# Performance work log

Hardware: AMD Instinct MI355X
Metric: run time of the kernel (lower is better)

## Reference

```python
import jax, jax.numpy as jnp
import numpy as np

TEMPERATURE = 8.0  # sqrt(d_k) with d_k = 64


def setup_inputs() -> dict:
    key = jax.random.key(0)
    k1, k2, k3, k4 = jax.random.split(key, 4)
    B, S, D = 16, 2048, 64  # B = batch * n_heads
    q = jax.random.normal(k1, (B, S, D), dtype=jnp.float32)
    k = jax.random.normal(k2, (B, S, D), dtype=jnp.float32)
    v = jax.random.normal(k3, (B, S, D), dtype=jnp.float32)
    # boolean mask: True = masked out. Low prob so no row is fully masked.
    mask = jax.random.uniform(k4, (B, S, S)) < 0.1
    return {"q": q, "k": k, "v": v, "mask": mask}


def reference(q, k, v, mask):
    # attn = (q @ k^T) / temperature, masked_fill(mask, -inf), softmax over last dim
    attn = jnp.einsum("bqd,bkd->bqk", q, k) / TEMPERATURE
    attn = jnp.where(mask, -jnp.inf, attn)
    attn = jax.nn.softmax(attn, axis=2)
    output = jnp.einsum("bqk,bkd->bqd", attn, v)
    return output, attn
```

## Files before the change

kernel.cpp:

```cpp
#include <hip/hip_runtime.h>

typedef _Float16 half8 __attribute__((ext_vector_type(8)));
typedef _Float16 half4 __attribute__((ext_vector_type(4)));
typedef float    floatx4 __attribute__((ext_vector_type(4)));
typedef int      intx4  __attribute__((ext_vector_type(4)));

#define NB  16
#define SEQ 2048
#define DIM 64

#define MFMA(a,b,c) __builtin_amdgcn_mfma_f32_16x16x32_f16((a),(b),(c),0,0,0)

__global__ __launch_bounds__(256) void cvt_qk_kernel(const float* __restrict__ q,
                                                     const float* __restrict__ k,
                                                     _Float16* __restrict__ qh,
                                                     _Float16* __restrict__ kh) {
    size_t i = ((size_t)blockIdx.x * 256 + threadIdx.x) * 4;
    float4 a = *(const float4*)(q + i);
    float4 b = *(const float4*)(k + i);
    half4 ha = { (_Float16)a.x, (_Float16)a.y, (_Float16)a.z, (_Float16)a.w };
    half4 hb = { (_Float16)b.x, (_Float16)b.y, (_Float16)b.z, (_Float16)b.w };
    *(half4*)(qh + i) = ha;
    *(half4*)(kh + i) = hb;
}

__global__ __launch_bounds__(256) void cvt_vt_kernel(const float* __restrict__ v,
                                                     _Float16* __restrict__ vt) {
    __shared__ float tile[64][65];
    const int b  = blockIdx.x >> 5;
    const int s0 = (blockIdx.x & 31) << 6;
    const int t  = threadIdx.x;
    {
        const int row = t >> 2;
        const int c0  = (t & 3) << 4;
        const float* src = v + ((size_t)(b * SEQ + s0 + row)) * DIM + c0;
        #pragma unroll
        for (int i = 0; i < 4; ++i) {
            float4 x = *(const float4*)(src + i * 4);
            tile[row][c0 + i*4 + 0] = x.x;
            tile[row][c0 + i*4 + 1] = x.y;
            tile[row][c0 + i*4 + 2] = x.z;
            tile[row][c0 + i*4 + 3] = x.w;
        }
    }
    __syncthreads();
    {
        const int d  = t >> 2;
        const int sb = (t & 3) << 4;
        _Float16* dst = vt + ((size_t)(b * DIM + d)) * SEQ + s0 + sb;
        #pragma unroll
        for (int i = 0; i < 4; ++i) {
            half4 h = { (_Float16)tile[sb + i*4 + 0][d],
                        (_Float16)tile[sb + i*4 + 1][d],
                        (_Float16)tile[sb + i*4 + 2][d],
                        (_Float16)tile[sb + i*4 + 3][d] };
            *(half4*)(dst + i*4) = h;
        }
    }
}

__global__ __launch_bounds__(256, 4) void attn_kernel(
    const _Float16* __restrict__ qh, const _Float16* __restrict__ kh,
    const _Float16* __restrict__ vt, const int* __restrict__ mask,
    float* __restrict__ out, float* __restrict__ attn)
{
    __shared__ float wsum[4][16];
    __shared__ __align__(16) _Float16 tsc[4][16][40];
    __shared__ __align__(16) float outred[4][16][68];

    const int b    = blockIdx.x >> 7;
    const int r0   = (blockIdx.x & 127) << 4;
    const int lane = threadIdx.x & 63;
    const int wave = threadIdx.x >> 6;
    const int rl   = lane & 15;
    const int g    = lane >> 4;

    const size_t qoff = ((size_t)(b * SEQ + r0 + rl)) * DIM + g * 8;
    const half8 qa0 = *(const half8*)(qh + qoff);
    const half8 qa1 = *(const half8*)(qh + qoff + 32);

    const _Float16* kbase = kh + (size_t)b * SEQ * DIM + (size_t)rl * DIM + g * 8;
    const int*      mbase = mask + ((size_t)(b * SEQ + r0 + rl)) * SEQ + g * 4;

    float rs = 0.f;
    uint32_t mb0 = 0, mb1 = 0, mb2 = 0, mb3 = 0;

    intx4 pm0 = __builtin_nontemporal_load((const intx4*)(mbase + wave * 32));
    intx4 pm1 = __builtin_nontemporal_load((const intx4*)(mbase + wave * 32 + 16));

    for (int cc = 0; cc < 16; ++cc) {
        const int jj = (cc * 4 + wave) * 32;
        const intx4 m0 = pm0, m1 = pm1;
        if (cc < 15) {
            pm0 = __builtin_nontemporal_load((const intx4*)(mbase + jj + 128));
            pm1 = __builtin_nontemporal_load((const intx4*)(mbase + jj + 128 + 16));
        }
        const _Float16* kp = kbase + (size_t)jj * DIM;
        half8 ka0 = *(const half8*)(kp);
        half8 ka1 = *(const half8*)(kp + 32);
        half8 kb0 = *(const half8*)(kp + 16 * DIM);
        half8 kb1 = *(const half8*)(kp + 16 * DIM + 32);
        floatx4 c0 = {0.f,0.f,0.f,0.f}, c1 = {0.f,0.f,0.f,0.f};
        c0 = MFMA(ka0, qa0, c0);
        c0 = MFMA(ka1, qa1, c0);
        c1 = MFMA(kb0, qa0, c1);
        c1 = MFMA(kb1, qa1, c1);
        float e0 = m0.x ? 0.f : __expf(c0[0] * 0.125f);
        float e1 = m0.y ? 0.f : __expf(c0[1] * 0.125f);
        float e2 = m0.z ? 0.f : __expf(c0[2] * 0.125f);
        float e3 = m0.w ? 0.f : __expf(c0[3] * 0.125f);
        float e4 = m1.x ? 0.f : __expf(c1[0] * 0.125f);
        float e5 = m1.y ? 0.f : __expf(c1[1] * 0.125f);
        float e6 = m1.z ? 0.f : __expf(c1[2] * 0.125f);
        float e7 = m1.w ? 0.f : __expf(c1[3] * 0.125f);
        rs += (e0 + e1) + (e2 + e3) + (e4 + e5) + (e6 + e7);
        uint32_t byt = (m0.x ? 1u : 0u)        | ((m0.y ? 1u : 0u) << 1)
                     | ((m0.z ? 1u : 0u) << 2) | ((m0.w ? 1u : 0u) << 3)
                     | ((m1.x ? 1u : 0u) << 4) | ((m1.y ? 1u : 0u) << 5)
                     | ((m1.z ? 1u : 0u) << 6) | ((m1.w ? 1u : 0u) << 7);
        mb0 = (mb0 >> 8) | (mb1 << 24);
        mb1 = (mb1 >> 8) | (mb2 << 24);
        mb2 = (mb2 >> 8) | (mb3 << 24);
        mb3 = (mb3 >> 8) | (byt << 24);
    }

    rs += __shfl_xor(rs, 16);
    rs += __shfl_xor(rs, 32);
    if (g == 0) wsum[wave][rl] = rs;
    __syncthreads();
    const float inv = 1.0f / (wsum[0][rl] + wsum[1][rl] + wsum[2][rl] + wsum[3][rl]);

    floatx4 o0 = {0.f,0.f,0.f,0.f}, o1 = {0.f,0.f,0.f,0.f};
    floatx4 o2 = {0.f,0.f,0.f,0.f}, o3 = {0.f,0.f,0.f,0.f};
    const _Float16* vbase = vt + ((size_t)b * DIM + rl) * SEQ + g * 8;
    float* abase = attn + ((size_t)(b * SEQ + r0 + rl)) * SEQ + g * 4;

    for (int cc = 0; cc < 16; ++cc) {
        const int jj = (cc * 4 + wave) * 32;
        const _Float16* kp = kbase + (size_t)jj * DIM;
        half8 ka0 = *(const half8*)(kp);
        half8 ka1 = *(const half8*)(kp + 32);
        half8 kb0 = *(const half8*)(kp + 16 * DIM);
        half8 kb1 = *(const half8*)(kp + 16 * DIM + 32);
        floatx4 c0 = {0.f,0.f,0.f,0.f}, c1 = {0.f,0.f,0.f,0.f};
        c0 = MFMA(ka0, qa0, c0);
        c0 = MFMA(ka1, qa1, c0);
        c1 = MFMA(kb0, qa0, c1);
        c1 = MFMA(kb1, qa1, c1);

        const uint32_t byt = mb0 & 0xffu;
        mb0 = (mb0 >> 8) | (mb1 << 24);
        mb1 = (mb1 >> 8) | (mb2 << 24);
        mb2 = (mb2 >> 8) | (mb3 << 24);
        mb3 =  mb3 >> 8;

        float e0 = (byt & 1u)   ? 0.f : __expf(c0[0] * 0.125f);
        float e1 = (byt & 2u)   ? 0.f : __expf(c0[1] * 0.125f);
        float e2 = (byt & 4u)   ? 0.f : __expf(c0[2] * 0.125f);
        float e3 = (byt & 8u)   ? 0.f : __expf(c0[3] * 0.125f);
        float e4 = (byt & 16u)  ? 0.f : __expf(c1[0] * 0.125f);
        float e5 = (byt & 32u)  ? 0.f : __expf(c1[1] * 0.125f);
        float e6 = (byt & 64u)  ? 0.f : __expf(c1[2] * 0.125f);
        float e7 = (byt & 128u) ? 0.f : __expf(c1[3] * 0.125f);

        floatx4 a0 = { e0 * inv, e1 * inv, e2 * inv, e3 * inv };
        floatx4 a1 = { e4 * inv, e5 * inv, e6 * inv, e7 * inv };
        __builtin_nontemporal_store(a0, (floatx4*)(abase + jj));
        __builtin_nontemporal_store(a1, (floatx4*)(abase + jj + 16));

        half4 h0 = { (_Float16)e0, (_Float16)e1, (_Float16)e2, (_Float16)e3 };
        half4 h1 = { (_Float16)e4, (_Float16)e5, (_Float16)e6, (_Float16)e7 };
        *(half4*)(&tsc[wave][rl][g * 4])      = h0;
        *(half4*)(&tsc[wave][rl][16 + g * 4]) = h1;
        half8 eb = *(const half8*)(&tsc[wave][rl][g * 8]);

        const _Float16* vp = vbase + jj;
        half8 v0 = *(const half8*)(vp);
        half8 v1 = *(const half8*)(vp + 16 * SEQ);
        half8 v2 = *(const half8*)(vp + 32 * SEQ);
        half8 v3 = *(const half8*)(vp + 48 * SEQ);
        o0 = MFMA(v0, eb, o0);
        o1 = MFMA(v1, eb, o1);
        o2 = MFMA(v2, eb, o2);
        o3 = MFMA(v3, eb, o3);
    }

    *(floatx4*)(&outred[wave][rl][ 0 + g * 4]) = o0;
    *(floatx4*)(&outred[wave][rl][16 + g * 4]) = o1;
    *(floatx4*)(&outred[wave][rl][32 + g * 4]) = o2;
    *(floatx4*)(&outred[wave][rl][48 + g * 4]) = o3;
    __syncthreads();
    {
        const int r  = threadIdx.x >> 4;
        const int c4 = (threadIdx.x & 15) << 2;
        floatx4 s0 = *(const floatx4*)(&outred[0][r][c4]);
        floatx4 s1 = *(const floatx4*)(&outred[1][r][c4]);
        floatx4 s2 = *(const floatx4*)(&outred[2][r][c4]);
        floatx4 s3 = *(const floatx4*)(&outred[3][r][c4]);
        floatx4 s = (s0 + s1) + (s2 + s3);
        const float inv2 = 1.0f / (wsum[0][r] + wsum[1][r] + wsum[2][r] + wsum[3][r]);
        floatx4 ov = { s[0] * inv2, s[1] * inv2, s[2] * inv2, s[3] * inv2 };
        *(floatx4*)(out + ((size_t)(b * SEQ + r0 + r)) * DIM + c4) = ov;
    }
}

extern "C" void kernel_launch(void* const* d_in, const int* in_sizes, int n_in,
                              void* d_out, int out_size, void* d_ws, size_t ws_size,
                              hipStream_t stream) {
    const float* q = (const float*)d_in[0];
    const float* k = (const float*)d_in[1];
    const float* v = (const float*)d_in[2];
    const int* mask = (const int*)d_in[3];

    float* out  = (float*)d_out;
    float* attn = out + (size_t)NB * SEQ * DIM;

    _Float16* qh = (_Float16*)d_ws;
    _Float16* kh = qh + (size_t)NB * SEQ * DIM;
    _Float16* vt = kh + (size_t)NB * SEQ * DIM;

    cvt_qk_kernel<<<(NB * SEQ * DIM) / 1024, 256, 0, stream>>>(q, k, qh, kh);
    cvt_vt_kernel<<<NB * (SEQ / 64), 256, 0, stream>>>(v, vt);
    attn_kernel<<<NB * (SEQ / 16), 256, 0, stream>>>(qh, kh, vt, mask, out, attn);
}
```

Measured before the change: 652.9 us.

## Pack mask into bitfields in a prepass and raise attention kernel occupancy

Adds a mask_bits_kernel that reads the int32 mask once and packs it with wave ballots into 32-bit words, one bit per key column. The attention kernel then reads those compact words in both passes, replacing the per-thread int4 mask loads and the register shift chain that carried mask bits from pass one to pass two. The attention kernel also aliases its two shared-memory arrays into one buffer, adding a barrier before reuse, so it can ask for 8 blocks per CU instead of 4. The attn stores switch from nontemporal to normal stores. The cost is an extra kernel launch and a separate full pass over the mask, and total mask traffic stays roughly the same.

```diff
diff --git a/kernel.cpp b/kernel.cpp
--- a/kernel.cpp
+++ b/kernel.cpp
@@ -3,7 +3,6 @@
 typedef _Float16 half8 __attribute__((ext_vector_type(8)));
 typedef _Float16 half4 __attribute__((ext_vector_type(4)));
 typedef float    floatx4 __attribute__((ext_vector_type(4)));
-typedef int      intx4  __attribute__((ext_vector_type(4)));
 
 #define NB  16
 #define SEQ 2048
@@ -59,14 +58,32 @@
     }
 }
 
-__global__ __launch_bounds__(256, 4) void attn_kernel(
+__global__ __launch_bounds__(256) void mask_bits_kernel(const int* __restrict__ mask,
+                                                        unsigned int* __restrict__ bits) {
+    const int wave = threadIdx.x >> 6;
+    const int lane = threadIdx.x & 63;
+    const size_t row = (size_t)blockIdx.x * 4 + wave;
+    const int* mp = mask + row * SEQ + lane;
+    unsigned int keep = 0;
+    #pragma unroll
+    for (int it = 0; it < 32; ++it) {
+        int m = __builtin_nontemporal_load(mp + it * 64);
+        unsigned long long bal = __ballot(m != 0);
+        unsigned int half = (lane & 1) ? (unsigned int)(bal >> 32) : (unsigned int)bal;
+        if ((lane >> 1) == it) keep = half;
+    }
+    bits[row * 64 + lane] = keep;
+}
+
+__global__ __launch_bounds__(256, 8) void attn_kernel(
     const _Float16* __restrict__ qh, const _Float16* __restrict__ kh,
-    const _Float16* __restrict__ vt, const int* __restrict__ mask,
+    const _Float16* __restrict__ vt, const unsigned int* __restrict__ bits,
     float* __restrict__ out, float* __restrict__ attn)
 {
     __shared__ float wsum[4][16];
-    __shared__ __align__(16) _Float16 tsc[4][16][40];
-    __shared__ __align__(16) float outred[4][16][68];
+    __shared__ __align__(16) unsigned char lds_u[4 * 16 * 68 * 4];
+    _Float16* tsc    = (_Float16*)lds_u;
+    float*    outred = (float*)lds_u;
 
     const int b    = blockIdx.x >> 7;
     const int r0   = (blockIdx.x & 127) << 4;
@@ -80,21 +97,15 @@
     const half8 qa1 = *(const half8*)(qh + qoff + 32);
 
     const _Float16* kbase = kh + (size_t)b * SEQ * DIM + (size_t)rl * DIM + g * 8;
-    const int*      mbase = mask + ((size_t)(b * SEQ + r0 + rl)) * SEQ + g * 4;
+    const unsigned int* bbase = bits + ((size_t)(b * SEQ + r0 + rl)) * 64 + wave;
 
     float rs = 0.f;
-    uint32_t mb0 = 0, mb1 = 0, mb2 = 0, mb3 = 0;
-
-    intx4 pm0 = __builtin_nontemporal_load((const intx4*)(mbase + wave * 32));
-    intx4 pm1 = __builtin_nontemporal_load((const intx4*)(mbase + wave * 32 + 16));
+    unsigned int pb = bbase[0];
 
     for (int cc = 0; cc < 16; ++cc) {
         const int jj = (cc * 4 + wave) * 32;
-        const intx4 m0 = pm0, m1 = pm1;
-        if (cc < 15) {
-            pm0 = __builtin_nontemporal_load((const intx4*)(mbase + jj + 128));
-            pm1 = __builtin_nontemporal_load((const intx4*)(mbase + jj + 128 + 16));
-        }
+        const unsigned int bm = pb;
+        if (cc < 15) pb = bbase[(cc + 1) * 4];
         const _Float16* kp = kbase + (size_t)jj * DIM;
         half8 ka0 = *(const half8*)(kp);
         half8 ka1 = *(const half8*)(kp + 32);
@@ -105,23 +116,17 @@
         c0 = MFMA(ka1, qa1, c0);
         c1 = MFMA(kb0, qa0, c1);
         c1 = MFMA(kb1, qa1, c1);
-        float e0 = m0.x ? 0.f : __expf(c0[0] * 0.125f);
-        float e1 = m0.y ? 0.f : __expf(c0[1] * 0.125f);
-        float e2 = m0.z ? 0.f : __expf(c0[2] * 0.125f);
-        float e3 = m0.w ? 0.f : __expf(c0[3] * 0.125f);
-        float e4 = m1.x ? 0.f : __expf(c1[0] * 0.125f);
-        float e5 = m1.y ? 0.f : __expf(c1[1] * 0.125f);
-        float e6 = m1.z ? 0.f : __expf(c1[2] * 0.125f);
-        float e7 = m1.w ? 0.f : __expf(c1[3] * 0.125f);
+        const unsigned int blo = bm >> (g * 4);
+        const unsigned int bhi = bm >> (g * 4 + 16);
+        float e0 = (blo & 1u) ? 0.f : __expf(c0[0] * 0.125f);
+        float e1 = (blo & 2u) ? 0.f : __expf(c0[1] * 0.125f);
+        float e2 = (blo & 4u) ? 0.f : __expf(c0[2] * 0.125f);
+        float e3 = (blo & 8u) ? 0.f : __expf(c0[3] * 0.125f);
+        float e4 = (bhi & 1u) ? 0.f : __expf(c1[0] * 0.125f);
+        float e5 = (bhi & 2u) ? 0.f : __expf(c1[1] * 0.125f);
+        float e6 = (bhi & 4u) ? 0.f : __expf(c1[2] * 0.125f);
+        float e7 = (bhi & 8u) ? 0.f : __expf(c1[3] * 0.125f);
         rs += (e0 + e1) + (e2 + e3) + (e4 + e5) + (e6 + e7);
-        uint32_t byt = (m0.x ? 1u : 0u)        | ((m0.y ? 1u : 0u) << 1)
-                     | ((m0.z ? 1u : 0u) << 2) | ((m0.w ? 1u : 0u) << 3)
-                     | ((m1.x ? 1u : 0u) << 4) | ((m1.y ? 1u : 0u) << 5)
-                     | ((m1.z ? 1u : 0u) << 6) | ((m1.w ? 1u : 0u) << 7);
-        mb0 = (mb0 >> 8) | (mb1 << 24);
-        mb1 = (mb1 >> 8) | (mb2 << 24);
-        mb2 = (mb2 >> 8) | (mb3 << 24);
-        mb3 = (mb3 >> 8) | (byt << 24);
     }
 
     rs += __shfl_xor(rs, 16);
@@ -134,9 +139,11 @@
     floatx4 o2 = {0.f,0.f,0.f,0.f}, o3 = {0.f,0.f,0.f,0.f};
     const _Float16* vbase = vt + ((size_t)b * DIM + rl) * SEQ + g * 8;
     float* abase = attn + ((size_t)(b * SEQ + r0 + rl)) * SEQ + g * 4;
+    _Float16* trow = tsc + (wave * 16 + rl) * 40;
 
     for (int cc = 0; cc < 16; ++cc) {
         const int jj = (cc * 4 + wave) * 32;
+        const unsigned int bm = bbase[cc * 4];
         const _Float16* kp = kbase + (size_t)jj * DIM;
         half8 ka0 = *(const half8*)(kp);
         half8 ka1 = *(const half8*)(kp + 32);
@@ -148,31 +155,27 @@
         c1 = MFMA(kb0, qa0, c1);
         c1 = MFMA(kb1, qa1, c1);
 
-        const uint32_t byt = mb0 & 0xffu;
-        mb0 = (mb0 >> 8) | (mb1 << 24);
-        mb1 = (mb1 >> 8) | (mb2 << 24);
-        mb2 = (mb2 >> 8) | (mb3 << 24);
-        mb3 =  mb3 >> 8;
-
-        float e0 = (byt & 1u)   ? 0.f : __expf(c0[0] * 0.125f);
-        float e1 = (byt & 2u)   ? 0.f : __expf(c0[1] * 0.125f);
-        float e2 = (byt & 4u)   ? 0.f : __expf(c0[2] * 0.125f);
-        float e3 = (byt & 8u)   ? 0.f : __expf(c0[3] * 0.125f);
-        float e4 = (byt & 16u)  ? 0.f : __expf(c1[0] * 0.125f);
-        float e5 = (byt & 32u)  ? 0.f : __expf(c1[1] * 0.125f);
-        float e6 = (byt & 64u)  ? 0.f : __expf(c1[2] * 0.125f);
-        float e7 = (byt & 128u) ? 0.f : __expf(c1[3] * 0.125f);
+        const unsigned int blo = bm >> (g * 4);
+        const unsigned int bhi = bm >> (g * 4 + 16);
+        float e0 = (blo & 1u) ? 0.f : __expf(c0[0] * 0.125f);
+        float e1 = (blo & 2u) ? 0.f : __expf(c0[1] * 0.125f);
+        float e2 = (blo & 4u) ? 0.f : __expf(c0[2] * 0.125f);
+        float e3 = (blo & 8u) ? 0.f : __expf(c0[3] * 0.125f);
+        float e4 = (bhi & 1u) ? 0.f : __expf(c1[0] * 0.125f);
+        float e5 = (bhi & 2u) ? 0.f : __expf(c1[1] * 0.125f);
+        float e6 = (bhi & 4u) ? 0.f : __expf(c1[2] * 0.125f);
+        float e7 = (bhi & 8u) ? 0.f : __expf(c1[3] * 0.125f);
 
         floatx4 a0 = { e0 * inv, e1 * inv, e2 * inv, e3 * inv };
         floatx4 a1 = { e4 * inv, e5 * inv, e6 * inv, e7 * inv };
-        __builtin_nontemporal_store(a0, (floatx4*)(abase + jj));
-        __builtin_nontemporal_store(a1, (floatx4*)(abase + jj + 16));
+        *(floatx4*)(abase + jj)      = a0;
+        *(floatx4*)(abase + jj + 16) = a1;
 
         half4 h0 = { (_Float16)e0, (_Float16)e1, (_Float16)e2, (_Float16)e3 };
         half4 h1 = { (_Float16)e4, (_Float16)e5, (_Float16)e6, (_Float16)e7 };
-        *(half4*)(&tsc[wave][rl][g * 4])      = h0;
-        *(half4*)(&tsc[wave][rl][16 + g * 4]) = h1;
-        half8 eb = *(const half8*)(&tsc[wave][rl][g * 8]);
+        *(half4*)(trow + g * 4)      = h0;
+        *(half4*)(trow + 16 + g * 4) = h1;
+        half8 eb = *(const half8*)(trow + g * 8);
 
         const _Float16* vp = vbase + jj;
         half8 v0 = *(const half8*)(vp);
@@ -185,18 +188,22 @@
         o3 = MFMA(v3, eb, o3);
     }
 
-    *(floatx4*)(&outred[wave][rl][ 0 + g * 4]) = o0;
-    *(floatx4*)(&outred[wave][rl][16 + g * 4]) = o1;
-    *(floatx4*)(&outred[wave][rl][32 + g * 4]) = o2;
-    *(floatx4*)(&outred[wave][rl][48 + g * 4]) = o3;
+    __syncthreads();
+    {
+        float* orow = outred + (wave * 16 + rl) * 68 + g * 4;
+        *(floatx4*)(orow +  0) = o0;
+        *(floatx4*)(orow + 16) = o1;
+        *(floatx4*)(orow + 32) = o2;
+        *(floatx4*)(orow + 48) = o3;
+    }
     __syncthreads();
     {
         const int r  = threadIdx.x >> 4;
         const int c4 = (threadIdx.x & 15) << 2;
-        floatx4 s0 = *(const floatx4*)(&outred[0][r][c4]);
-        floatx4 s1 = *(const floatx4*)(&outred[1][r][c4]);
-        floatx4 s2 = *(const floatx4*)(&outred[2][r][c4]);
-        floatx4 s3 = *(const floatx4*)(&outred[3][r][c4]);
+        floatx4 s0 = *(const floatx4*)(outred + ( 0 + r) * 68 + c4);
+        floatx4 s1 = *(const floatx4*)(outred + (16 + r) * 68 + c4);
+        floatx4 s2 = *(const floatx4*)(outred + (32 + r) * 68 + c4);
+        floatx4 s3 = *(const floatx4*)(outred + (48 + r) * 68 + c4);
         floatx4 s = (s0 + s1) + (s2 + s3);
         const float inv2 = 1.0f / (wsum[0][r] + wsum[1][r] + wsum[2][r] + wsum[3][r]);
         floatx4 ov = { s[0] * inv2, s[1] * inv2, s[2] * inv2, s[3] * inv2 };
@@ -218,8 +225,10 @@
     _Float16* qh = (_Float16*)d_ws;
     _Float16* kh = qh + (size_t)NB * SEQ * DIM;
     _Float16* vt = kh + (size_t)NB * SEQ * DIM;
+    unsigned int* bits = (unsigned int*)(vt + (size_t)NB * SEQ * DIM);
 
     cvt_qk_kernel<<<(NB * SEQ * DIM) / 1024, 256, 0, stream>>>(q, k, qh, kh);
     cvt_vt_kernel<<<NB * (SEQ / 64), 256, 0, stream>>>(v, vt);
-    attn_kernel<<<NB * (SEQ / 16), 256, 0, stream>>>(qh, kh, vt, mask, out, attn);
-}
+    mask_bits_kernel<<<(NB * SEQ) / 4, 256, 0, stream>>>(mask, bits);
+    attn_kernel<<<NB * (SEQ / 16), 256, 0, stream>>>(qh, kh, vt, bits, out, attn);
+}
```

New measurement: 623.8 us. -4.5%, faster.
